# Kernel optimization log

Measured on AMD Instinct MI355X. Metric: run time of the kernel, lower is better.

The kernel has to match this reference:

```python
import jax, jax.numpy as jnp
import numpy as np

B = 1024      # batch
D_NUM = 100   # numeric features
N_CAT = 20    # categorical features
CARD = 100    # cardinality per categorical feature
D = 1024      # d_token
DH = 675      # int(d_token * 0.66)
NT = D_NUM + 1 + N_CAT  # 121 tokens (CLS + numeric + categorical)
E = 4         # num_experts
K = 2         # top_k
MID = 512     # ResidualHead mid dim = max(D//2, 16)
RH = 256      # router/alpha hidden = max(D//4, 16)


def _ln(x, g, b):
    m = x.mean(-1, keepdims=True)
    v = ((x - m) ** 2).mean(-1, keepdims=True)
    return (x - m) * jax.lax.rsqrt(v + 1e-5) * g + b


def setup_inputs() -> dict:
    key = jax.random.key(0)
    ks = jax.random.split(key, 20)

    def n(i, shape, s=0.02):
        return jax.random.normal(ks[i], shape, dtype=jnp.float32) * s

    return dict(
        x_num=jax.random.normal(ks[0], (B, D_NUM), dtype=jnp.float32),
        x_cat=jax.random.randint(ks[1], (B, N_CAT), 0, CARD),
        tok_w=n(2, (D_NUM + 1, D), 0.05),
        tok_b=n(3, (D_NUM + N_CAT, D), 0.05),
        cat_emb=n(4, (N_CAT * CARD, D), 0.05),
        ln_g=jnp.ones((D,), jnp.float32), ln_b=jnp.zeros((D,), jnp.float32),
        lin0_w=n(5, (D, 2 * DH)), lin0_b=jnp.zeros((2 * DH,), jnp.float32),
        sgu_ln_g=jnp.ones((DH,), jnp.float32), sgu_ln_b=jnp.zeros((DH,), jnp.float32),
        sgu_w=n(6, (NT, NT), 0.05), sgu_b=jnp.zeros((NT,), jnp.float32),
        lin1_w=n(7, (DH, D)), lin1_b=jnp.zeros((D,), jnp.float32),
        r_w1=n(8, (D, RH)), r_b1=jnp.zeros((RH,), jnp.float32),
        r_w2=n(9, (RH, E)), r_b2=jnp.zeros((E,), jnp.float32),
        a_w1=n(10, (D, RH)), a_b1=jnp.zeros((RH,), jnp.float32),
        a_w2=n(11, (RH, 1)), a_b2=jnp.full((1,), -4.0, jnp.float32),
        base_w=n(12, (D, 1)), base_b=jnp.zeros((1,), jnp.float32),
        gh_w1=n(13, (D, MID), 0.001), gh_b1=jnp.zeros((MID,), jnp.float32),
        gh_w2=n(14, (MID, 1), 0.001), gh_b2=jnp.zeros((1,), jnp.float32),
        ex_w1=n(15, (E, D, MID), 0.001), ex_b1=jnp.zeros((E, MID), jnp.float32),
        ex_w2=n(16, (E, MID), 0.001), ex_b2=jnp.zeros((E,), jnp.float32),
    )


def reference(x_num, x_cat, tok_w, tok_b, cat_emb, ln_g, ln_b, lin0_w, lin0_b,
              sgu_ln_g, sgu_ln_b, sgu_w, sgu_b, lin1_w, lin1_b,
              r_w1, r_b1, r_w2, r_b2, a_w1, a_b1, a_w2, a_b2,
              base_w, base_b, gh_w1, gh_b1, gh_w2, gh_b2,
              ex_w1, ex_b1, ex_w2, ex_b2):
    # ---- Tokenizer ----
    offsets = jnp.arange(N_CAT) * CARD
    xn = jnp.concatenate([jnp.ones((x_num.shape[0], 1), x_num.dtype), x_num], axis=1)  # [B, D_NUM+1]
    x = tok_w[None] * xn[:, :, None]                                  # [B, D_NUM+1, D]
    x = jnp.concatenate([x, cat_emb[x_cat + offsets[None]]], axis=1)  # [B, NT, D]
    bias_full = jnp.concatenate([jnp.zeros((1, D), tok_b.dtype), tok_b], axis=0)
    x = x + bias_full[None]
    # ---- gMLP layer (n_layers=1) ----
    xr = x
    h = _ln(x, ln_g, ln_b)
    h = jax.nn.gelu(h @ lin0_w + lin0_b, approximate=False)           # [B, NT, 2*DH]
    u, v = h[..., :DH], h[..., DH:]
    v = _ln(v, sgu_ln_g, sgu_ln_b)
    # SGU token-mixing: out[b,s,d] = sum_t v[b,t,d] * W[s,t] + bias[s]
    v = jnp.einsum('btd,st->bsd', v, sgu_w) + sgu_b[None, :, None]
    x = (u * v) @ lin1_w + lin1_b
    x = x + xr
    # ---- pooled hidden (CLS token) ----
    hidden = jax.nn.gelu(_ln(x[:, 0], ln_g, ln_b), approximate=False)  # [B, D]
    # ---- router + top-k sparsification ----
    logits = jax.nn.relu(hidden @ r_w1 + r_b1) @ r_w2 + r_b2           # [B, E]
    dense = jax.nn.softmax(logits, axis=-1)
    vals, idx = jax.lax.top_k(dense, K)
    sparse = jnp.zeros_like(dense).at[jnp.arange(dense.shape[0])[:, None], idx].set(vals)
    rw = sparse / jnp.clip(sparse.sum(-1, keepdims=True), 1e-8)
    # ---- local experts (small residual heads, vectorized over E) ----
    eh = jax.nn.relu(jnp.einsum('bd,edm->bem', hidden, ex_w1) + ex_b1[None])
    eo = jnp.einsum('bem,em->be', eh, ex_w2) + ex_b2[None]             # [B, E]
    local = (rw * eo).sum(-1, keepdims=True)                           # [B, 1]
    # ---- global residual, alpha gate, base head ----
    glob = jax.nn.relu(hidden @ gh_w1 + gh_b1) @ gh_w2 + gh_b2
    alpha = jax.nn.sigmoid(jax.nn.relu(hidden @ a_w1 + a_b1) @ a_w2 + a_b2)
    y_base = hidden @ base_w + base_b
    return y_base + alpha * (glob + local)                             # [B, 1]
```

## Files before the change

kernel.cpp:

```cpp
#include <hip/hip_runtime.h>
#include <math.h>

#define B_SZ 1024

typedef __attribute__((ext_vector_type(8))) short bf16x8;
typedef __attribute__((ext_vector_type(4))) float f32x4;
typedef __attribute__((ext_vector_type(4))) float floatx4;
typedef __attribute__((ext_vector_type(4))) unsigned short ushortx4;

#define GLOAD16(src, dst) __builtin_amdgcn_global_load_lds( \
    (const __attribute__((address_space(1))) void*)(src), \
    (__attribute__((address_space(3))) void*)(dst), 16, 0, 0)

__device__ __forceinline__ unsigned short f2bf(float f) {
  unsigned int u = __float_as_uint(f);
  u += 0x7fff + ((u >> 16) & 1);
  return (unsigned short)(u >> 16);
}
__device__ __forceinline__ float bf2f(unsigned short b) {
  return __uint_as_float(((unsigned int)b) << 16);
}
__device__ __forceinline__ float gelu_exact(float x) {
  return 0.5f * x * (1.0f + erff(x * 0.70710678118654752f));
}
__device__ __forceinline__ float gelu_fast(float x) {
  const float c0 = 2.3022586f;
  const float c1 = 0.10295465f;
  float z = x * __builtin_fmaf(x * x, c1, c0);
  float e = __builtin_amdgcn_exp2f(z);
  float r = __builtin_amdgcn_rcpf(e + 1.0f);
  return __builtin_fmaf(-x, r, x);
}
__device__ __forceinline__ float wred(float v) {
#pragma unroll
  for (int o = 32; o > 0; o >>= 1) v += __shfl_xor(v, o, 64);
  return v;
}

struct PrepArgs {
  const float* src[10];
  unsigned short* dst[10];
  int ldin[10]; int coff[10]; int Nsrc[10]; int Ksrc[10]; int Kp[10];
  int nbx[10]; int blk0[11];
};

__global__ __launch_bounds__(256)
void prep_all(PrepArgs J,
              const float* __restrict__ tok_w, const float* __restrict__ tok_b,
              const float* __restrict__ cat_emb,
              const float* __restrict__ ln_g, const float* __restrict__ ln_b,
              const float* __restrict__ r_b1, const float* __restrict__ a_b1,
              const float* __restrict__ gh_b1, const float* __restrict__ ex_b1,
              unsigned short* __restrict__ Amat,
              float* __restrict__ nstat, float* __restrict__ cstat,
              float* __restrict__ bcat)
{
  const int bid = blockIdx.x;
  const int tid = threadIdx.x;
  const int lane = tid & 63;
  const int NT = J.blk0[10];
  if (bid < NT) {
    __shared__ float tile[64][65];
    int j = 0;
    while (bid >= J.blk0[j + 1]) ++j;
    const int bx = bid - J.blk0[j];
    const int k0 = (bx % J.nbx[j]) * 64;
    const int n0 = (bx / J.nbx[j]) * 64;
    const float* in = J.src[j];
    unsigned short* out = J.dst[j];
    const int ldin = J.ldin[j], coff = J.coff[j], Nsrc = J.Nsrc[j], Ksrc = J.Ksrc[j], Kp = J.Kp[j];
    const int kx = tid & 63;
    const int ry = tid >> 6;
    for (int r = ry; r < 64; r += 4) {
      const int k = k0 + r;
      const int n = n0 + kx;
      tile[r][kx] = (k < Ksrc && n < Nsrc) ? in[(size_t)k * ldin + coff + n] : 0.f;
    }
    __syncthreads();
    for (int r = ry; r < 64; r += 4) {
      const int n = n0 + r;
      const int k = k0 + kx;
      out[(size_t)n * Kp + k] = f2bf(tile[kx][r]);
    }
  } else if (bid < NT + 576) {
    const int r = (bid - NT) * 4 + (tid >> 6);
    if (r >= 2304) return;
    unsigned short* out = Amat + (size_t)r * 1024;
    for (int k = lane * 4; k < 1024; k += 256) {
      floatx4 g = *(const floatx4*)(ln_g + k);
      floatx4 v;
      if (r <= 100) {
        floatx4 a = *(const floatx4*)(tok_w + (size_t)r * 1024 + k);
#pragma unroll
        for (int q = 0; q < 4; q++) v[q] = a[q] * g[q];
      } else if (r <= 200) {
        floatx4 a = *(const floatx4*)(tok_b + (size_t)(r - 101) * 1024 + k);
#pragma unroll
        for (int q = 0; q < 4; q++) v[q] = a[q] * g[q];
      } else if (r <= 2200) {
        const int j = r - 201;
        const int c = j / 100;
        floatx4 a = *(const floatx4*)(cat_emb + (size_t)j * 1024 + k);
        floatx4 bq = *(const floatx4*)(tok_b + (size_t)(100 + c) * 1024 + k);
#pragma unroll
        for (int q = 0; q < 4; q++) v[q] = (a[q] + bq[q]) * g[q];
      } else if (r == 2201) {
        v = g;
      } else if (r == 2202) {
        v = *(const floatx4*)(ln_b + k);
      } else {
        v[0] = 0.f; v[1] = 0.f; v[2] = 0.f; v[3] = 0.f;
      }
      ushortx4 o;
#pragma unroll
      for (int q = 0; q < 4; q++) o[q] = f2bf(v[q]);
      *(ushortx4*)(out + k) = o;
    }
  } else if (bid < NT + 576 + 526) {
    const int w = (bid - NT - 576) * 4 + (tid >> 6);
    if (w >= 2101) return;
    if (w <= 100) {
      const int t = w;
      const float* wr = tok_w + (size_t)t * 1024;
      const float* br = (t >= 1) ? (tok_b + (size_t)(t - 1) * 1024) : nullptr;
      float sw = 0, sww = 0, sb = 0, sbb = 0, swb = 0;
      for (int k = lane * 4; k < 1024; k += 256) {
        floatx4 a = *(const floatx4*)(wr + k);
#pragma unroll
        for (int q = 0; q < 4; q++) { sw += a[q]; sww += a[q] * a[q]; }
        if (br) {
          floatx4 bq = *(const floatx4*)(br + k);
#pragma unroll
          for (int q = 0; q < 4; q++) { sb += bq[q]; sbb += bq[q] * bq[q]; swb += a[q] * bq[q]; }
        }
      }
      sw = wred(sw); sww = wred(sww); sb = wred(sb); sbb = wred(sbb); swb = wred(swb);
      if (lane == 0) {
        float* ns = nstat + (size_t)t * 5;
        ns[0] = sw; ns[1] = sww; ns[2] = sb; ns[3] = sbb; ns[4] = swb;
      }
    } else {
      const int j = w - 101;
      const int c = j / 100;
      const float* ar = cat_emb + (size_t)j * 1024;
      const float* br = tok_b + (size_t)(100 + c) * 1024;
      float s1 = 0, s2 = 0;
      for (int k = lane * 4; k < 1024; k += 256) {
        floatx4 a = *(const floatx4*)(ar + k);
        floatx4 bq = *(const floatx4*)(br + k);
#pragma unroll
        for (int q = 0; q < 4; q++) { const float v = a[q] + bq[q]; s1 += v; s2 += v * v; }
      }
      s1 = wred(s1); s2 = wred(s2);
      if (lane == 0) { cstat[(size_t)j * 2] = s1; cstat[(size_t)j * 2 + 1] = s2; }
    }
  } else {
    const int n = (bid - NT - 1102) * 256 + tid;
    if (n >= 3072) return;
    float v;
    if (n < 256) v = r_b1[n];
    else if (n < 512) v = a_b1[n - 256];
    else if (n < 1024) v = gh_b1[n - 512];
    else v = ex_b1[n - 1024];
    bcat[n] = v;
  }
}

template<int EPI>
__device__ __forceinline__
void gemm_body(int bid, const unsigned short* __restrict__ A, long pitchA,
               const unsigned short* __restrict__ Bw, int K,
               const float* __restrict__ bias, int bias_off,
               const float* __restrict__ extra,
               int NB, int Nvalid, int ldo,
               float* __restrict__ outf, unsigned short* __restrict__ outb)
{
  __shared__ unsigned short As[128 * 32];
  __shared__ unsigned short Bs[128 * 32];
  const int tid = threadIdx.x, lane = tid & 63, wv = tid >> 6;
  const int nb = bid % NB, mb = bid / NB;
  const int m0 = mb * 128, n0 = nb * 128;
  const int wr = (wv >> 1) << 6, wc = (wv & 1) << 6;
  const int fr = lane & 15, fq = lane >> 4;
  const int c0 = wv * 2;
  const int srow = lane >> 2;
  const int sk = (lane & 3) << 3;

  const unsigned short* a0 = A + (size_t)(m0 + c0 * 16 + srow) * pitchA + sk;
  const unsigned short* a1 = A + (size_t)(m0 + (c0 + 1) * 16 + srow) * pitchA + sk;
  const unsigned short* b0p = Bw + (size_t)(n0 + c0 * 16 + srow) * K + sk;
  const unsigned short* b1p = Bw + (size_t)(n0 + (c0 + 1) * 16 + srow) * K + sk;

  f32x4 acc[4][4] = {};
  for (int k0 = 0; k0 < K; k0 += 32) {
    __syncthreads();
    GLOAD16(a0 + k0, &As[c0 * 512]);
    GLOAD16(a1 + k0, &As[(c0 + 1) * 512]);
    GLOAD16(b0p + k0, &Bs[c0 * 512]);
    GLOAD16(b1p + k0, &Bs[(c0 + 1) * 512]);
    __syncthreads();
    bf16x8 af[4], bw_[4];
#pragma unroll
    for (int i = 0; i < 4; i++) {
      af[i]  = *(const bf16x8*)&As[(wr + i * 16 + fr) * 32 + fq * 8];
      bw_[i] = *(const bf16x8*)&Bs[(wc + i * 16 + fr) * 32 + fq * 8];
    }
#pragma unroll
    for (int i = 0; i < 4; i++)
#pragma unroll
      for (int j = 0; j < 4; j++)
        acc[i][j] = __builtin_amdgcn_mfma_f32_16x16x32_bf16(af[i], bw_[j], acc[i][j], 0, 0, 0);
  }

#pragma unroll
  for (int i = 0; i < 4; i++)
#pragma unroll
    for (int j = 0; j < 4; j++) {
      const int n = n0 + wc + j * 16 + fr;
      if (n >= ldo) continue;
      const bool valid = (n < Nvalid);
      const float bv = (EPI == 3) ? 0.f : (valid ? bias[bias_off + n] : 0.f);
      const float ev = (EPI == 0) ? extra[n] : 0.f;
#pragma unroll
      for (int q = 0; q < 4; q++) {
        const int m = m0 + wr + i * 16 + fq * 4 + q;
        const float a = acc[i][j][q];
        if (EPI == 0) {
          outf[(size_t)m * ldo + n] = a + bv + ev;
        } else if (EPI == 1) {
          outb[(size_t)m * ldo + n] = f2bf(fmaxf(a + bv, 0.f));
        } else {
          outf[(size_t)m * ldo + n] = a;
        }
      }
    }
}

template<int EPI>
__global__ __launch_bounds__(256)
void gemm_gl(const unsigned short* __restrict__ A, long pitchA,
             const unsigned short* __restrict__ Bw, int K,
             const float* __restrict__ bias, int bias_off,
             const float* __restrict__ extra,
             int NB, int Nvalid, int ldo,
             float* __restrict__ outf, unsigned short* __restrict__ outb)
{
  gemm_body<EPI>(blockIdx.x, A, pitchA, Bw, K, bias, bias_off, extra, NB, Nvalid, ldo, outf, outb);
}

__device__ __forceinline__
void u_const_body(int bid, const unsigned short* __restrict__ w0u, const float* __restrict__ nstat,
                  const float* __restrict__ tok_w, const float* __restrict__ ln_g,
                  const float* __restrict__ ln_b, const float* __restrict__ lin0_b,
                  float* __restrict__ ucon)
{
  __shared__ float xk[1024];
  const int tid = threadIdx.x, lane = tid & 63, wv = tid >> 6;
  const float m = nstat[0] * (1.f / 1024.f);
  const float ex2 = nstat[1] * (1.f / 1024.f);
  const float rs = rsqrtf(ex2 - m * m + 1e-5f);
  for (int k = tid; k < 1024; k += 256)
    xk[k] = bf2f(f2bf((tok_w[k] - m) * rs * ln_g[k] + ln_b[k]));
  __syncthreads();
  const int c = bid * 4 + wv;
  if (c >= 704) return;
  if (c >= 675) { if (lane == 0) ucon[c] = 0.f; return; }
  const unsigned short* wr = w0u + (size_t)c * 1024;
  float s = 0.f;
  for (int k = lane; k < 1024; k += 64) s += bf2f(wr[k]) * xk[k];
  s = wred(s);
  if (lane == 0) ucon[c] = gelu_exact(s + lin0_b[c]);
}

__global__ __launch_bounds__(256)
void tab_and_u(const unsigned short* __restrict__ Amat, const unsigned short* __restrict__ w0v,
               float* __restrict__ TAB,
               const unsigned short* __restrict__ w0u, const float* __restrict__ nstat,
               const float* __restrict__ tok_w, const float* __restrict__ ln_g,
               const float* __restrict__ ln_b, const float* __restrict__ lin0_b,
               float* __restrict__ ucon)
{
  if (blockIdx.x < 108)
    gemm_body<3>(blockIdx.x, Amat, 1024, w0v, 1024, nullptr, 0, nullptr, 6, 768, 768, TAB, nullptr);
  else
    u_const_body(blockIdx.x - 108, w0u, nstat, tok_w, ln_g, ln_b, lin0_b, ucon);
}

__global__ __launch_bounds__(256)
void cat_rows(const float* __restrict__ TAB, const float* __restrict__ nstat,
              const float* __restrict__ cstat, const float* __restrict__ lin0_b,
              float* __restrict__ catval, float* __restrict__ catsc)
{
  const int r = blockIdx.x * 4 + (threadIdx.x >> 6);
  const int lane = threadIdx.x & 63;
  if (r >= 2001) return;
  float m, ex2;
  const float* T1;
  if (r < 2000) {
    m = cstat[(size_t)r * 2] * (1.f / 1024.f);
    ex2 = cstat[(size_t)r * 2 + 1] * (1.f / 1024.f);
    T1 = TAB + (size_t)(201 + r) * 768;
  } else {
    m = nstat[0] * (1.f / 1024.f);
    ex2 = nstat[1] * (1.f / 1024.f);
    T1 = TAB;
  }
  const float rs = rsqrtf(ex2 - m * m + 1e-5f);
  const float ga = -m * rs;
  const float* R = TAB + (size_t)2201 * 768;
  const float* C = TAB + (size_t)2202 * 768;
  const int dl = lane << 2;
  float s = 0.f, ss = 0.f;
  float* outp = catval + (size_t)r * 768;
#pragma unroll
  for (int ch = 0; ch < 3; ch++) {
    const int d = ch * 256 + dl;
    floatx4 t1 = *(const floatx4*)(T1 + d);
    floatx4 rr = *(const floatx4*)(R + d);
    floatx4 cc = *(const floatx4*)(C + d);
    floatx4 o;
#pragma unroll
    for (int q = 0; q < 4; q++) {
      const int dd = d + q;
      const float c2 = (dd < 675) ? (cc[q] + lin0_b[675 + dd]) : 0.f;
      const float pre = __builtin_fmaf(rs, t1[q], __builtin_fmaf(ga, rr[q], c2));
      const float g = (dd < 675) ? gelu_fast(pre) : 0.f;
      o[q] = g; s += g; ss = __builtin_fmaf(g, g, ss);
    }
    *(floatx4*)(outp + d) = o;
  }
  s = wred(s); ss = wred(ss);
  const float mu = s * (1.f / 675.f);
  const float rho = rsqrtf(ss * (1.f / 675.f) - mu * mu + 1e-5f);
  if (lane == 0) { catsc[(size_t)r * 2] = mu; catsc[(size_t)r * 2 + 1] = rho; }
}

__global__ __launch_bounds__(512)
void fused_v2(const float* __restrict__ TAB, const float* __restrict__ nstat,
              const float* __restrict__ catsc, const float* __restrict__ catval,
              const float* __restrict__ x_num, const int* __restrict__ x_cat,
              const float* __restrict__ sgu_ln_g, const float* __restrict__ sgu_ln_b,
              const float* __restrict__ sgu_w, const float* __restrict__ sgu_b,
              const float* __restrict__ lin0_b, const float* __restrict__ ucon,
              unsigned short* __restrict__ uv)
{
  const int b0 = blockIdx.x, b1 = blockIdx.x + 512;
  const int tid = threadIdx.x, lane = tid & 63, wv = tid >> 6;
  __shared__ float Rls[768], Cls[768];
  __shared__ float alf[2][100], bet[2][100], gam[2][100], swt[100];
  __shared__ float wrc[2][21], catkb[2][21];
  __shared__ int catrowS[2][21];
  __shared__ float accw[8][768];
  __shared__ float kbw[2][8];
  __shared__ float wss_s;

  for (int d = tid; d < 768; d += 512) {
    Rls[d] = (d < 675) ? TAB[(size_t)2201 * 768 + d] : 0.f;
    Cls[d] = (d < 675) ? (TAB[(size_t)2202 * 768 + d] + lin0_b[675 + d]) : 0.f;
  }
  if (tid < 200) {
    const int bb = tid / 100, tt = tid % 100;
    const int b = bb ? b1 : b0;
    const float sc = x_num[b * 100 + tt];
    const float* ns = nstat + (size_t)(tt + 1) * 5;
    const float m = (sc * ns[0] + ns[2]) * (1.f / 1024.f);
    const float ex2 = (sc * sc * ns[1] + 2.f * sc * ns[4] + ns[3]) * (1.f / 1024.f);
    const float rs = rsqrtf(ex2 - m * m + 1e-5f);
    alf[bb][tt] = rs * sc; bet[bb][tt] = rs; gam[bb][tt] = -m * rs;
    if (bb == 0) swt[tt] = sgu_w[tt + 1];
  } else if (tid < 242) {
    const int idx = tid - 200;
    const int bb = idx / 21, ii = idx % 21;
    const int b = bb ? b1 : b0;
    int row; float sw;
    if (ii < 20) { row = x_cat[b * 20 + ii] + 100 * ii; sw = sgu_w[101 + ii]; }
    else { row = 2000; sw = sgu_w[0]; }
    const float mu = catsc[(size_t)row * 2], rho = catsc[(size_t)row * 2 + 1];
    const float wr = sw * rho;
    wrc[bb][ii] = wr; catkb[bb][ii] = wr * mu; catrowS[bb][ii] = row;
  } else if (tid >= 256 && tid < 320) {
    float s = (lane < 121 ? sgu_w[lane] : 0.f) + (lane + 64 < 121 ? sgu_w[lane + 64] : 0.f);
    s = wred(s);
    if (lane == 0) wss_s = s;
  }
  __syncthreads();

  float accA[12] = {}, accB[12] = {};
  float kbA = 0.f, kbB = 0.f;
  const int dl = lane << 2;

  for (int i = 0; i < 13; i++) {
    const int tt = wv + 8 * i;
    if (tt >= 100) break;
    const float a0 = alf[0][tt], be0 = bet[0][tt], ga0 = gam[0][tt];
    const float a1 = alf[1][tt], be1 = bet[1][tt], ga1 = gam[1][tt];
    const float* T1 = TAB + (size_t)(tt + 1) * 768;
    const float* T2 = TAB + (size_t)(101 + tt) * 768;
    float s0 = 0.f, ss0 = 0.f, s1 = 0.f, ss1 = 0.f;
    float va[12], vb[12];
#pragma unroll
    for (int ch = 0; ch < 3; ch++) {
      const int d = ch * 256 + dl;
      floatx4 t1 = *(const floatx4*)(T1 + d);
      floatx4 t2 = *(const floatx4*)(T2 + d);
      floatx4 rr = *(const floatx4*)(&Rls[d]);
      floatx4 cc = *(const floatx4*)(&Cls[d]);
#pragma unroll
      for (int q = 0; q < 4; q++) {
        const float pre0 = __builtin_fmaf(a0, t1[q], __builtin_fmaf(be0, t2[q], __builtin_fmaf(ga0, rr[q], cc[q])));
        const float g0 = gelu_fast(pre0);
        va[ch * 4 + q] = g0; s0 += g0; ss0 = __builtin_fmaf(g0, g0, ss0);
        const float pre1 = __builtin_fmaf(a1, t1[q], __builtin_fmaf(be1, t2[q], __builtin_fmaf(ga1, rr[q], cc[q])));
        const float g1 = gelu_fast(pre1);
        vb[ch * 4 + q] = g1; s1 += g1; ss1 = __builtin_fmaf(g1, g1, ss1);
      }
    }
    s0 = wred(s0); ss0 = wred(ss0); s1 = wred(s1); ss1 = wred(ss1);
    const float sw = swt[tt];
    const float mu0 = s0 * (1.f / 675.f);
    const float rho0 = rsqrtf(ss0 * (1.f / 675.f) - mu0 * mu0 + 1e-5f);
    const float w0 = sw * rho0;
    const float mu1 = s1 * (1.f / 675.f);
    const float rho1 = rsqrtf(ss1 * (1.f / 675.f) - mu1 * mu1 + 1e-5f);
    const float w1 = sw * rho1;
#pragma unroll
    for (int q = 0; q < 12; q++) {
      accA[q] = __builtin_fmaf(w0, va[q], accA[q]);
      accB[q] = __builtin_fmaf(w1, vb[q], accB[q]);
    }
    kbA = __builtin_fmaf(w0, mu0, kbA);
    kbB = __builtin_fmaf(w1, mu1, kbB);
  }

  for (int i = 0; i < 3; i++) {
    const int ii = wv + 8 * i;
    if (ii >= 21) break;
    {
      const float wr = wrc[0][ii];
      const float* cv = catval + (size_t)catrowS[0][ii] * 768;
#pragma unroll
      for (int ch = 0; ch < 3; ch++) {
        floatx4 v = *(const floatx4*)(cv + ch * 256 + dl);
#pragma unroll
        for (int q = 0; q < 4; q++) accA[ch * 4 + q] = __builtin_fmaf(wr, v[q], accA[ch * 4 + q]);
      }
    }
    {
      const float wr = wrc[1][ii];
      const float* cv = catval + (size_t)catrowS[1][ii] * 768;
#pragma unroll
      for (int ch = 0; ch < 3; ch++) {
        floatx4 v = *(const floatx4*)(cv + ch * 256 + dl);
#pragma unroll
        for (int q = 0; q < 4; q++) accB[ch * 4 + q] = __builtin_fmaf(wr, v[q], accB[ch * 4 + q]);
      }
    }
  }
  if (lane == 0) { kbw[0][wv] = kbA; kbw[1][wv] = kbB; }

  const float sb0 = sgu_b[0];

#pragma unroll
  for (int ch = 0; ch < 3; ch++)
    *(floatx4*)&accw[wv][ch * 256 + dl] = *(const floatx4*)&accA[ch * 4];
  __syncthreads();
  {
    float kbs = 0.f;
#pragma unroll
    for (int w = 0; w < 8; w++) kbs += kbw[0][w];
#pragma unroll
    for (int i = 0; i < 21; i++) kbs += catkb[0][i];
    const float wss = wss_s;
    for (int d = tid; d < 704; d += 512) {
      unsigned short o = 0;
      if (d < 675) {
        float a = 0.f;
#pragma unroll
        for (int w = 0; w < 8; w++) a += accw[w][d];
        const float v0 = sgu_ln_g[d] * (a - kbs) + sgu_ln_b[d] * wss + sb0;
        o = f2bf(ucon[d] * v0);
      }
      uv[(size_t)b0 * 704 + d] = o;
    }
  }
  __syncthreads();
#pragma unroll
  for (int ch = 0; ch < 3; ch++)
    *(floatx4*)&accw[wv][ch * 256 + dl] = *(const floatx4*)&accB[ch * 4];
  __syncthreads();
  {
    float kbs = 0.f;
#pragma unroll
    for (int w = 0; w < 8; w++) kbs += kbw[1][w];
#pragma unroll
    for (int i = 0; i < 21; i++) kbs += catkb[1][i];
    const float wss = wss_s;
    for (int d = tid; d < 704; d += 512) {
      unsigned short o = 0;
      if (d < 675) {
        float a = 0.f;
#pragma unroll
        for (int w = 0; w < 8; w++) a += accw[w][d];
        const float v0 = sgu_ln_g[d] * (a - kbs) + sgu_ln_b[d] * wss + sb0;
        o = f2bf(ucon[d] * v0);
      }
      uv[(size_t)b1 * 704 + d] = o;
    }
  }
}

__global__ __launch_bounds__(256)
void ln_gelu_hidden(const float* __restrict__ xfin,
                    const float* __restrict__ ln_g, const float* __restrict__ ln_b,
                    float* __restrict__ hid_f, unsigned short* __restrict__ hid_bf)
{
  const int w = (blockIdx.x * 256 + threadIdx.x) >> 6;
  const int lane = threadIdx.x & 63;
  if (w >= B_SZ) return;
  const float* row = xfin + (size_t)w * 1024;
  float s = 0.f, ss = 0.f;
  for (int k = lane; k < 1024; k += 64) { float v = row[k]; s += v; ss += v * v; }
  s = wred(s); ss = wred(ss);
  const float m = s * (1.f / 1024.f);
  const float var = ss * (1.f / 1024.f) - m * m;
  const float rs = rsqrtf(var + 1e-5f);
  for (int k = lane; k < 1024; k += 64) {
    float v = gelu_exact((row[k] - m) * rs * ln_g[k] + ln_b[k]);
    hid_f[(size_t)w * 1024 + k] = v;
    hid_bf[(size_t)w * 1024 + k] = f2bf(v);
  }
}

__global__ __launch_bounds__(256)
void final_head(const unsigned short* __restrict__ H1, const float* __restrict__ hid_f,
                const float* __restrict__ r_w2, const float* __restrict__ r_b2,
                const float* __restrict__ a_w2, const float* __restrict__ a_b2,
                const float* __restrict__ gh_w2, const float* __restrict__ gh_b2,
                const float* __restrict__ ex_w2, const float* __restrict__ ex_b2,
                const float* __restrict__ base_w, const float* __restrict__ base_b,
                float* __restrict__ out)
{
  const int b = blockIdx.x;
  const int tid = threadIdx.x;
  const unsigned short* h1 = H1 + (size_t)b * 3072;
  float p[11];
#pragma unroll
  for (int i = 0; i < 11; i++) p[i] = 0.f;
  {
    const int m = tid;
    const float hr = bf2f(h1[m]);
    p[0] = hr * r_w2[m * 4 + 0];
    p[1] = hr * r_w2[m * 4 + 1];
    p[2] = hr * r_w2[m * 4 + 2];
    p[3] = hr * r_w2[m * 4 + 3];
    const float ha = bf2f(h1[256 + m]);
    p[4] = ha * a_w2[m];
  }
  for (int m = tid; m < 512; m += 256) {
    p[5] += bf2f(h1[512 + m]) * gh_w2[m];
#pragma unroll
    for (int e = 0; e < 4; e++)
      p[6 + e] += bf2f(h1[1024 + e * 512 + m]) * ex_w2[e * 512 + m];
  }
  for (int k = tid; k < 1024; k += 256) p[10] += hid_f[(size_t)b * 1024 + k] * base_w[k];

  __shared__ float red[11][4];
  const int lane = tid & 63, wv = tid >> 6;
#pragma unroll
  for (int i = 0; i < 11; i++) {
    const float v = wred(p[i]);
    if (lane == 0) red[i][wv] = v;
  }
  __syncthreads();
  if (tid == 0) {
    float s[11];
#pragma unroll
    for (int i = 0; i < 11; i++) s[i] = red[i][0] + red[i][1] + red[i][2] + red[i][3];
    float lg[4];
#pragma unroll
    for (int e = 0; e < 4; e++) lg[e] = s[e] + r_b2[e];
    const float mx = fmaxf(fmaxf(lg[0], lg[1]), fmaxf(lg[2], lg[3]));
    float den[4]; float dsum = 0.f;
#pragma unroll
    for (int e = 0; e < 4; e++) { den[e] = expf(lg[e] - mx); dsum += den[e]; }
#pragma unroll
    for (int e = 0; e < 4; e++) den[e] /= dsum;
    int i1 = 0;
    for (int e = 1; e < 4; e++) if (den[e] > den[i1]) i1 = e;
    int i2 = -1;
    for (int e = 0; e < 4; e++) { if (e == i1) continue; if (i2 < 0 || den[e] > den[i2]) i2 = e; }
    float eo[4];
#pragma unroll
    for (int e = 0; e < 4; e++) eo[e] = s[6 + e] + ex_b2[e];
    const float v1 = den[i1], v2 = den[i2];
    const float ssum = fmaxf(v1 + v2, 1e-8f);
    const float local = (v1 * eo[i1] + v2 * eo[i2]) / ssum;
    const float glob = s[5] + gh_b2[0];
    const float alpha = 1.0f / (1.0f + expf(-(s[4] + a_b2[0])));
    out[b] = s[10] + base_b[0] + alpha * (glob + local);
  }
}

extern "C" void kernel_launch(void* const* d_in, const int* in_sizes, int n_in,
                              void* d_out, int out_size, void* d_ws, size_t ws_size,
                              hipStream_t stream)
{
  const float* x_num  = (const float*)d_in[0];
  const int*   x_cat  = (const int*)d_in[1];
  const float* tok_w  = (const float*)d_in[2];
  const float* tok_b  = (const float*)d_in[3];
  const float* cat_emb= (const float*)d_in[4];
  const float* ln_g   = (const float*)d_in[5];
  const float* ln_b   = (const float*)d_in[6];
  const float* lin0_w = (const float*)d_in[7];
  const float* lin0_b = (const float*)d_in[8];
  const float* sgu_ln_g = (const float*)d_in[9];
  const float* sgu_ln_b = (const float*)d_in[10];
  const float* sgu_w  = (const float*)d_in[11];
  const float* sgu_b  = (const float*)d_in[12];
  const float* lin1_w = (const float*)d_in[13];
  const float* lin1_b = (const float*)d_in[14];
  const float* r_w1   = (const float*)d_in[15];
  const float* r_b1   = (const float*)d_in[16];
  const float* r_w2   = (const float*)d_in[17];
  const float* r_b2   = (const float*)d_in[18];
  const float* a_w1   = (const float*)d_in[19];
  const float* a_b1   = (const float*)d_in[20];
  const float* a_w2   = (const float*)d_in[21];
  const float* a_b2   = (const float*)d_in[22];
  const float* base_w = (const float*)d_in[23];
  const float* base_b = (const float*)d_in[24];
  const float* gh_w1  = (const float*)d_in[25];
  const float* gh_b1  = (const float*)d_in[26];
  const float* gh_w2  = (const float*)d_in[27];
  const float* gh_b2  = (const float*)d_in[28];
  const float* ex_w1  = (const float*)d_in[29];
  const float* ex_b1  = (const float*)d_in[30];
  const float* ex_w2  = (const float*)d_in[31];
  const float* ex_b2  = (const float*)d_in[32];
  (void)in_sizes; (void)n_in; (void)out_size; (void)ws_size;

  char* ws = (char*)d_ws;
  size_t off = 0;
  auto alloc = [&](size_t bytes) { void* p = ws + off; off += (bytes + 255) & ~(size_t)255; return p; };

  unsigned short* w0v  = (unsigned short*)alloc((size_t)768 * 1024 * 2);
  unsigned short* w0u  = (unsigned short*)alloc((size_t)768 * 1024 * 2);
  unsigned short* w1t  = (unsigned short*)alloc((size_t)1024 * 704 * 2);
  unsigned short* wcat = (unsigned short*)alloc((size_t)3072 * 1024 * 2);
  float* bcat          = (float*)alloc((size_t)3072 * 4);
  unsigned short* Amat = (unsigned short*)alloc((size_t)2304 * 1024 * 2);
  float* TAB           = (float*)alloc((size_t)2304 * 768 * 4);
  float* nstat         = (float*)alloc((size_t)101 * 5 * 4);
  float* cstat         = (float*)alloc((size_t)2000 * 2 * 4);
  float* catval        = (float*)alloc((size_t)2001 * 768 * 4);
  float* catsc         = (float*)alloc((size_t)2001 * 2 * 4);
  float* ucon          = (float*)alloc((size_t)704 * 4);
  unsigned short* uv   = (unsigned short*)alloc((size_t)B_SZ * 704 * 2);
  float* xfin          = (float*)alloc((size_t)B_SZ * 1024 * 4);
  float* hid_f         = (float*)alloc((size_t)B_SZ * 1024 * 4);
  unsigned short* hidb = (unsigned short*)alloc((size_t)B_SZ * 1024 * 2);
  unsigned short* H1   = (unsigned short*)alloc((size_t)B_SZ * 3072 * 2);

  const dim3 blk(256);

  PrepArgs J;
  auto setJ = [&](int i, const float* s, unsigned short* d, int ldin, int coff,
                  int Nsrc, int Ksrc, int Kp, int nbx, int nby) {
    J.src[i] = s; J.dst[i] = d; J.ldin[i] = ldin; J.coff[i] = coff;
    J.Nsrc[i] = Nsrc; J.Ksrc[i] = Ksrc; J.Kp[i] = Kp; J.nbx[i] = nbx;
    J.blk0[i + 1] = J.blk0[i] + nbx * nby;
  };
  J.blk0[0] = 0;
  setJ(0, lin0_w, w0v, 1350, 675, 675, 1024, 1024, 16, 12);
  setJ(1, lin0_w, w0u, 1350, 0,   675, 1024, 1024, 16, 12);
  setJ(2, lin1_w, w1t, 1024, 0,  1024,  675,  704, 11, 16);
  setJ(3, r_w1,  wcat,                          256, 0, 256, 1024, 1024, 16, 4);
  setJ(4, a_w1,  wcat + (size_t)256 * 1024,     256, 0, 256, 1024, 1024, 16, 4);
  setJ(5, gh_w1, wcat + (size_t)512 * 1024,     512, 0, 512, 1024, 1024, 16, 8);
  for (int e = 0; e < 4; e++)
    setJ(6 + e, ex_w1 + (size_t)e * 1024 * 512,
         wcat + (size_t)(1024 + e * 512) * 1024, 512, 0, 512, 1024, 1024, 16, 8);

  const int nprep = J.blk0[10] + 576 + 526 + 12;
  prep_all<<<nprep, blk, 0, stream>>>(J, tok_w, tok_b, cat_emb, ln_g, ln_b,
      r_b1, a_b1, gh_b1, ex_b1, Amat, nstat, cstat, bcat);

  tab_and_u<<<284, blk, 0, stream>>>(Amat, w0v, TAB, w0u, nstat, tok_w, ln_g, ln_b, lin0_b, ucon);

  cat_rows<<<501, blk, 0, stream>>>(TAB, nstat, cstat, lin0_b, catval, catsc);

  fused_v2<<<512, dim3(512), 0, stream>>>(TAB, nstat, catsc, catval, x_num, x_cat,
      sgu_ln_g, sgu_ln_b, sgu_w, sgu_b, lin0_b, ucon, uv);

  gemm_gl<0><<<8 * 8, blk, 0, stream>>>(uv, 704, w1t, 704,
      lin1_b, 0, tok_w, 8, 1024, 1024, xfin, nullptr);
  ln_gelu_hidden<<<B_SZ / 4, blk, 0, stream>>>(xfin, ln_g, ln_b, hid_f, hidb);
  gemm_gl<1><<<8 * 24, blk, 0, stream>>>(hidb, 1024, wcat, 1024,
      bcat, 0, nullptr, 24, 3072, 3072, nullptr, H1);

  final_head<<<B_SZ, blk, 0, stream>>>(H1, hid_f, r_w2, r_b2, a_w2, a_b2, gh_w2, gh_b2,
                                       ex_w2, ex_b2, base_w, base_b, (float*)d_out);
}
```

Measured before the change: 152.1 us.

## Use 64x64 GEMM tiles, drop w0u prep, fuse base head into LN-GELU

Shrinks the MFMA GEMM tile from 128x128 to 64x64 so the three GEMMs launch 4x more blocks and fill more of the GPU's compute units. The separate bf16 transpose of the u-half of lin0_w is removed. The u-constant vector is now computed directly from the fp32 weights, with a column-parallel split-K reduction. The base head dot product moves into the LN-GELU kernel, which also switches to the fast GELU approximation, so the fp32 hidden buffer is no longer written or re-read. Smaller tiles lower data reuse per block, and the fast GELU adds approximation error to the hidden values.

```diff
diff --git a/kernel.cpp b/kernel.cpp
--- a/kernel.cpp
+++ b/kernel.cpp
@@ -38,10 +38,10 @@
 }
 
 struct PrepArgs {
-  const float* src[10];
-  unsigned short* dst[10];
-  int ldin[10]; int coff[10]; int Nsrc[10]; int Ksrc[10]; int Kp[10];
-  int nbx[10]; int blk0[11];
+  const float* src[9];
+  unsigned short* dst[9];
+  int ldin[9]; int coff[9]; int Nsrc[9]; int Ksrc[9]; int Kp[9];
+  int nbx[9]; int blk0[10];
 };
 
 __global__ __launch_bounds__(256)
@@ -58,7 +58,7 @@
   const int bid = blockIdx.x;
   const int tid = threadIdx.x;
   const int lane = tid & 63;
-  const int NT = J.blk0[10];
+  const int NT = J.blk0[9];
   if (bid < NT) {
     __shared__ float tile[64][65];
     int j = 0;
@@ -168,58 +168,50 @@
 
 template<int EPI>
 __device__ __forceinline__
-void gemm_body(int bid, const unsigned short* __restrict__ A, long pitchA,
-               const unsigned short* __restrict__ Bw, int K,
-               const float* __restrict__ bias, int bias_off,
-               const float* __restrict__ extra,
-               int NB, int Nvalid, int ldo,
-               float* __restrict__ outf, unsigned short* __restrict__ outb)
-{
-  __shared__ unsigned short As[128 * 32];
-  __shared__ unsigned short Bs[128 * 32];
+void gemm64_body(int bid, const unsigned short* __restrict__ A, long pitchA,
+                 const unsigned short* __restrict__ Bw, int K,
+                 const float* __restrict__ bias, const float* __restrict__ extra,
+                 int NB, int Nvalid, int ldo,
+                 float* __restrict__ outf, unsigned short* __restrict__ outb)
+{
+  __shared__ unsigned short As[64 * 32];
+  __shared__ unsigned short Bs[64 * 32];
   const int tid = threadIdx.x, lane = tid & 63, wv = tid >> 6;
   const int nb = bid % NB, mb = bid / NB;
-  const int m0 = mb * 128, n0 = nb * 128;
-  const int wr = (wv >> 1) << 6, wc = (wv & 1) << 6;
+  const int m0 = mb * 64, n0 = nb * 64;
+  const int wr = (wv >> 1) << 5, wc = (wv & 1) << 5;
   const int fr = lane & 15, fq = lane >> 4;
-  const int c0 = wv * 2;
-  const int srow = lane >> 2;
-  const int sk = (lane & 3) << 3;
-
-  const unsigned short* a0 = A + (size_t)(m0 + c0 * 16 + srow) * pitchA + sk;
-  const unsigned short* a1 = A + (size_t)(m0 + (c0 + 1) * 16 + srow) * pitchA + sk;
-  const unsigned short* b0p = Bw + (size_t)(n0 + c0 * 16 + srow) * K + sk;
-  const unsigned short* b1p = Bw + (size_t)(n0 + (c0 + 1) * 16 + srow) * K + sk;
-
-  f32x4 acc[4][4] = {};
+
+  const unsigned short* srcA = A + (size_t)(m0 + (tid >> 2)) * pitchA + ((tid & 3) << 3);
+  const unsigned short* srcB = Bw + (size_t)(n0 + (tid >> 2)) * K + ((tid & 3) << 3);
+
+  f32x4 acc[2][2] = {};
   for (int k0 = 0; k0 < K; k0 += 32) {
     __syncthreads();
-    GLOAD16(a0 + k0, &As[c0 * 512]);
-    GLOAD16(a1 + k0, &As[(c0 + 1) * 512]);
-    GLOAD16(b0p + k0, &Bs[c0 * 512]);
-    GLOAD16(b1p + k0, &Bs[(c0 + 1) * 512]);
+    GLOAD16(srcA + k0, &As[tid * 8]);
+    GLOAD16(srcB + k0, &Bs[tid * 8]);
     __syncthreads();
-    bf16x8 af[4], bw_[4];
-#pragma unroll
-    for (int i = 0; i < 4; i++) {
+    bf16x8 af[2], bw_[2];
+#pragma unroll
+    for (int i = 0; i < 2; i++) {
       af[i]  = *(const bf16x8*)&As[(wr + i * 16 + fr) * 32 + fq * 8];
       bw_[i] = *(const bf16x8*)&Bs[(wc + i * 16 + fr) * 32 + fq * 8];
     }
 #pragma unroll
-    for (int i = 0; i < 4; i++)
-#pragma unroll
-      for (int j = 0; j < 4; j++)
+    for (int i = 0; i < 2; i++)
+#pragma unroll
+      for (int j = 0; j < 2; j++)
         acc[i][j] = __builtin_amdgcn_mfma_f32_16x16x32_bf16(af[i], bw_[j], acc[i][j], 0, 0, 0);
   }
 
 #pragma unroll
-  for (int i = 0; i < 4; i++)
-#pragma unroll
-    for (int j = 0; j < 4; j++) {
+  for (int i = 0; i < 2; i++)
+#pragma unroll
+    for (int j = 0; j < 2; j++) {
       const int n = n0 + wc + j * 16 + fr;
       if (n >= ldo) continue;
       const bool valid = (n < Nvalid);
-      const float bv = (EPI == 3) ? 0.f : (valid ? bias[bias_off + n] : 0.f);
+      const float bv = (EPI == 3) ? 0.f : (valid ? bias[n] : 0.f);
       const float ev = (EPI == 0) ? extra[n] : 0.f;
 #pragma unroll
       for (int q = 0; q < 4; q++) {
@@ -238,52 +230,58 @@
 
 template<int EPI>
 __global__ __launch_bounds__(256)
-void gemm_gl(const unsigned short* __restrict__ A, long pitchA,
-             const unsigned short* __restrict__ Bw, int K,
-             const float* __restrict__ bias, int bias_off,
-             const float* __restrict__ extra,
-             int NB, int Nvalid, int ldo,
-             float* __restrict__ outf, unsigned short* __restrict__ outb)
-{
-  gemm_body<EPI>(blockIdx.x, A, pitchA, Bw, K, bias, bias_off, extra, NB, Nvalid, ldo, outf, outb);
+void gemm64(const unsigned short* __restrict__ A, long pitchA,
+            const unsigned short* __restrict__ Bw, int K,
+            const float* __restrict__ bias, const float* __restrict__ extra,
+            int NB, int Nvalid, int ldo,
+            float* __restrict__ outf, unsigned short* __restrict__ outb)
+{
+  gemm64_body<EPI>(blockIdx.x, A, pitchA, Bw, K, bias, extra, NB, Nvalid, ldo, outf, outb);
 }
 
 __device__ __forceinline__
-void u_const_body(int bid, const unsigned short* __restrict__ w0u, const float* __restrict__ nstat,
-                  const float* __restrict__ tok_w, const float* __restrict__ ln_g,
-                  const float* __restrict__ ln_b, const float* __restrict__ lin0_b,
-                  float* __restrict__ ucon)
+void ucon_body(int bid, const float* __restrict__ lin0_w, const float* __restrict__ nstat,
+               const float* __restrict__ tok_w, const float* __restrict__ ln_g,
+               const float* __restrict__ ln_b, const float* __restrict__ lin0_b,
+               float* __restrict__ ucon)
 {
   __shared__ float xk[1024];
-  const int tid = threadIdx.x, lane = tid & 63, wv = tid >> 6;
+  __shared__ float part[4][64];
+  const int tid = threadIdx.x;
   const float m = nstat[0] * (1.f / 1024.f);
   const float ex2 = nstat[1] * (1.f / 1024.f);
   const float rs = rsqrtf(ex2 - m * m + 1e-5f);
   for (int k = tid; k < 1024; k += 256)
     xk[k] = bf2f(f2bf((tok_w[k] - m) * rs * ln_g[k] + ln_b[k]));
   __syncthreads();
-  const int c = bid * 4 + wv;
-  if (c >= 704) return;
-  if (c >= 675) { if (lane == 0) ucon[c] = 0.f; return; }
-  const unsigned short* wr = w0u + (size_t)c * 1024;
-  float s = 0.f;
-  for (int k = lane; k < 1024; k += 64) s += bf2f(wr[k]) * xk[k];
-  s = wred(s);
-  if (lane == 0) ucon[c] = gelu_exact(s + lin0_b[c]);
+  const int c = bid * 64 + (tid & 63);
+  const int ks = tid >> 6;
+  float acc = 0.f;
+  for (int k = ks * 256; k < ks * 256 + 256; k++)
+    acc = __builtin_fmaf(xk[k], bf2f(f2bf(lin0_w[(size_t)k * 1350 + c])), acc);
+  part[ks][tid & 63] = acc;
+  __syncthreads();
+  if (tid < 64) {
+    const int cc = bid * 64 + tid;
+    if (cc < 704) {
+      const float s = part[0][tid] + part[1][tid] + part[2][tid] + part[3][tid];
+      ucon[cc] = (cc < 675) ? gelu_exact(s + lin0_b[cc]) : 0.f;
+    }
+  }
 }
 
 __global__ __launch_bounds__(256)
 void tab_and_u(const unsigned short* __restrict__ Amat, const unsigned short* __restrict__ w0v,
                float* __restrict__ TAB,
-               const unsigned short* __restrict__ w0u, const float* __restrict__ nstat,
+               const float* __restrict__ lin0_w, const float* __restrict__ nstat,
                const float* __restrict__ tok_w, const float* __restrict__ ln_g,
                const float* __restrict__ ln_b, const float* __restrict__ lin0_b,
                float* __restrict__ ucon)
 {
-  if (blockIdx.x < 108)
-    gemm_body<3>(blockIdx.x, Amat, 1024, w0v, 1024, nullptr, 0, nullptr, 6, 768, 768, TAB, nullptr);
+  if (blockIdx.x < 432)
+    gemm64_body<3>(blockIdx.x, Amat, 1024, w0v, 1024, nullptr, nullptr, 12, 768, 768, TAB, nullptr);
   else
-    u_const_body(blockIdx.x - 108, w0u, nstat, tok_w, ln_g, ln_b, lin0_b, ucon);
+    ucon_body(blockIdx.x - 432, lin0_w, nstat, tok_w, ln_g, ln_b, lin0_b, ucon);
 }
 
 __global__ __launch_bounds__(256)
@@ -512,7 +510,8 @@
 __global__ __launch_bounds__(256)
 void ln_gelu_hidden(const float* __restrict__ xfin,
                     const float* __restrict__ ln_g, const float* __restrict__ ln_b,
-                    float* __restrict__ hid_f, unsigned short* __restrict__ hid_bf)
+                    const float* __restrict__ base_w,
+                    unsigned short* __restrict__ hid_bf, float* __restrict__ base_y)
 {
   const int w = (blockIdx.x * 256 + threadIdx.x) >> 6;
   const int lane = threadIdx.x & 63;
@@ -524,28 +523,31 @@
   const float m = s * (1.f / 1024.f);
   const float var = ss * (1.f / 1024.f) - m * m;
   const float rs = rsqrtf(var + 1e-5f);
+  float bacc = 0.f;
   for (int k = lane; k < 1024; k += 64) {
-    float v = gelu_exact((row[k] - m) * rs * ln_g[k] + ln_b[k]);
-    hid_f[(size_t)w * 1024 + k] = v;
+    float v = gelu_fast((row[k] - m) * rs * ln_g[k] + ln_b[k]);
     hid_bf[(size_t)w * 1024 + k] = f2bf(v);
-  }
+    bacc = __builtin_fmaf(v, base_w[k], bacc);
+  }
+  bacc = wred(bacc);
+  if (lane == 0) base_y[w] = bacc;
 }
 
 __global__ __launch_bounds__(256)
-void final_head(const unsigned short* __restrict__ H1, const float* __restrict__ hid_f,
+void final_head(const unsigned short* __restrict__ H1, const float* __restrict__ base_y,
                 const float* __restrict__ r_w2, const float* __restrict__ r_b2,
                 const float* __restrict__ a_w2, const float* __restrict__ a_b2,
                 const float* __restrict__ gh_w2, const float* __restrict__ gh_b2,
                 const float* __restrict__ ex_w2, const float* __restrict__ ex_b2,
-                const float* __restrict__ base_w, const float* __restrict__ base_b,
+                const float* __restrict__ base_b,
                 float* __restrict__ out)
 {
   const int b = blockIdx.x;
   const int tid = threadIdx.x;
   const unsigned short* h1 = H1 + (size_t)b * 3072;
-  float p[11];
-#pragma unroll
-  for (int i = 0; i < 11; i++) p[i] = 0.f;
+  float p[10];
+#pragma unroll
+  for (int i = 0; i < 10; i++) p[i] = 0.f;
   {
     const int m = tid;
     const float hr = bf2f(h1[m]);
@@ -562,20 +564,19 @@
     for (int e = 0; e < 4; e++)
       p[6 + e] += bf2f(h1[1024 + e * 512 + m]) * ex_w2[e * 512 + m];
   }
-  for (int k = tid; k < 1024; k += 256) p[10] += hid_f[(size_t)b * 1024 + k] * base_w[k];
-
-  __shared__ float red[11][4];
+
+  __shared__ float red[10][4];
   const int lane = tid & 63, wv = tid >> 6;
 #pragma unroll
-  for (int i = 0; i < 11; i++) {
+  for (int i = 0; i < 10; i++) {
     const float v = wred(p[i]);
     if (lane == 0) red[i][wv] = v;
   }
   __syncthreads();
   if (tid == 0) {
-    float s[11];
-#pragma unroll
-    for (int i = 0; i < 11; i++) s[i] = red[i][0] + red[i][1] + red[i][2] + red[i][3];
+    float s[10];
+#pragma unroll
+    for (int i = 0; i < 10; i++) s[i] = red[i][0] + red[i][1] + red[i][2] + red[i][3];
     float lg[4];
 #pragma unroll
     for (int e = 0; e < 4; e++) lg[e] = s[e] + r_b2[e];
@@ -597,7 +598,7 @@
     const float local = (v1 * eo[i1] + v2 * eo[i2]) / ssum;
     const float glob = s[5] + gh_b2[0];
     const float alpha = 1.0f / (1.0f + expf(-(s[4] + a_b2[0])));
-    out[b] = s[10] + base_b[0] + alpha * (glob + local);
+    out[b] = base_y[b] + base_b[0] + alpha * (glob + local);
   }
 }
 
@@ -645,7 +646,6 @@
   auto alloc = [&](size_t bytes) { void* p = ws + off; off += (bytes + 255) & ~(size_t)255; return p; };
 
   unsigned short* w0v  = (unsigned short*)alloc((size_t)768 * 1024 * 2);
-  unsigned short* w0u  = (unsigned short*)alloc((size_t)768 * 1024 * 2);
   unsigned short* w1t  = (unsigned short*)alloc((size_t)1024 * 704 * 2);
   unsigned short* wcat = (unsigned short*)alloc((size_t)3072 * 1024 * 2);
   float* bcat          = (float*)alloc((size_t)3072 * 4);
@@ -658,7 +658,7 @@
   float* ucon          = (float*)alloc((size_t)704 * 4);
   unsigned short* uv   = (unsigned short*)alloc((size_t)B_SZ * 704 * 2);
   float* xfin          = (float*)alloc((size_t)B_SZ * 1024 * 4);
-  float* hid_f         = (float*)alloc((size_t)B_SZ * 1024 * 4);
+  float* base_y        = (float*)alloc((size_t)B_SZ * 4);
   unsigned short* hidb = (unsigned short*)alloc((size_t)B_SZ * 1024 * 2);
   unsigned short* H1   = (unsigned short*)alloc((size_t)B_SZ * 3072 * 2);
 
@@ -673,32 +673,31 @@
   };
   J.blk0[0] = 0;
   setJ(0, lin0_w, w0v, 1350, 675, 675, 1024, 1024, 16, 12);
-  setJ(1, lin0_w, w0u, 1350, 0,   675, 1024, 1024, 16, 12);
-  setJ(2, lin1_w, w1t, 1024, 0,  1024,  675,  704, 11, 16);
-  setJ(3, r_w1,  wcat,                          256, 0, 256, 1024, 1024, 16, 4);
-  setJ(4, a_w1,  wcat + (size_t)256 * 1024,     256, 0, 256, 1024, 1024, 16, 4);
-  setJ(5, gh_w1, wcat + (size_t)512 * 1024,     512, 0, 512, 1024, 1024, 16, 8);
+  setJ(1, lin1_w, w1t, 1024, 0,  1024,  675,  704, 11, 16);
+  setJ(2, r_w1,  wcat,                          256, 0, 256, 1024, 1024, 16, 4);
+  setJ(3, a_w1,  wcat + (size_t)256 * 1024,     256, 0, 256, 1024, 1024, 16, 4);
+  setJ(4, gh_w1, wcat + (size_t)512 * 1024,     512, 0, 512, 1024, 1024, 16, 8);
   for (int e = 0; e < 4; e++)
-    setJ(6 + e, ex_w1 + (size_t)e * 1024 * 512,
+    setJ(5 + e, ex_w1 + (size_t)e * 1024 * 512,
          wcat + (size_t)(1024 + e * 512) * 1024, 512, 0, 512, 1024, 1024, 16, 8);
 
-  const int nprep = J.blk0[10] + 576 + 526 + 12;
+  const int nprep = J.blk0[9] + 576 + 526 + 12;
   prep_all<<<nprep, blk, 0, stream>>>(J, tok_w, tok_b, cat_emb, ln_g, ln_b,
       r_b1, a_b1, gh_b1, ex_b1, Amat, nstat, cstat, bcat);
 
-  tab_and_u<<<284, blk, 0, stream>>>(Amat, w0v, TAB, w0u, nstat, tok_w, ln_g, ln_b, lin0_b, ucon);
+  tab_and_u<<<443, blk, 0, stream>>>(Amat, w0v, TAB, lin0_w, nstat, tok_w, ln_g, ln_b, lin0_b, ucon);
 
   cat_rows<<<501, blk, 0, stream>>>(TAB, nstat, cstat, lin0_b, catval, catsc);
 
   fused_v2<<<512, dim3(512), 0, stream>>>(TAB, nstat, catsc, catval, x_num, x_cat,
       sgu_ln_g, sgu_ln_b, sgu_w, sgu_b, lin0_b, ucon, uv);
 
-  gemm_gl<0><<<8 * 8, blk, 0, stream>>>(uv, 704, w1t, 704,
-      lin1_b, 0, tok_w, 8, 1024, 1024, xfin, nullptr);
-  ln_gelu_hidden<<<B_SZ / 4, blk, 0, stream>>>(xfin, ln_g, ln_b, hid_f, hidb);
-  gemm_gl<1><<<8 * 24, blk, 0, stream>>>(hidb, 1024, wcat, 1024,
-      bcat, 0, nullptr, 24, 3072, 3072, nullptr, H1);
-
-  final_head<<<B_SZ, blk, 0, stream>>>(H1, hid_f, r_w2, r_b2, a_w2, a_b2, gh_w2, gh_b2,
-                                       ex_w2, ex_b2, base_w, base_b, (float*)d_out);
-}
+  gemm64<0><<<16 * 16, blk, 0, stream>>>(uv, 704, w1t, 704,
+      lin1_b, tok_w, 16, 1024, 1024, xfin, nullptr);
+  ln_gelu_hidden<<<B_SZ / 4, blk, 0, stream>>>(xfin, ln_g, ln_b, base_w, hidb, base_y);
+  gemm64<1><<<16 * 48, blk, 0, stream>>>(hidb, 1024, wcat, 1024,
+      bcat, nullptr, 48, 3072, 3072, nullptr, H1);
+
+  final_head<<<B_SZ, blk, 0, stream>>>(H1, base_y, r_w2, r_b2, a_w2, a_b2, gh_w2, gh_b2,
+                                       ex_w2, ex_b2, base_b, (float*)d_out);
+}
```

New measurement: 139.7 us. 1.09x faster.
